# Performance work log

Hardware: AMD Instinct MI355X
Metric: run time of the kernel (lower is better)

## Reference

```python
import jax, jax.numpy as jnp
import numpy as np

N, E = 20000, 320000
EPS = 1e-5
NEG_SLOPE = 0.2


def gat_conv(x, src, dst, W, att_src, att_dst, bias, num_nodes):
    # W: [Fin, H*C], att_*: [H, C], bias: [H*C]
    H, C = att_src.shape
    h = (x @ W).reshape(num_nodes, H, C)            # [N,H,C]
    a_s = jnp.einsum('nhc,hc->nh', h, att_src)      # [N,H]
    a_d = jnp.einsum('nhc,hc->nh', h, att_dst)      # [N,H]
    e = jax.nn.leaky_relu(a_s[src] + a_d[dst], NEG_SLOPE)  # [E,H]
    m = jax.ops.segment_max(e, dst, num_segments=num_nodes)       # per-dst max (self-loops guarantee non-empty)
    ex = jnp.exp(e - m[dst])
    s = jax.ops.segment_sum(ex, dst, num_segments=num_nodes)
    alpha = ex / s[dst]                              # [E,H] segment softmax
    out = jax.ops.segment_sum(h[src] * alpha[:, :, None], dst, num_segments=num_nodes)  # [N,H,C]
    return out.reshape(num_nodes, H * C) + bias


def batch_norm(x, gamma, beta):
    mu = x.mean(axis=0)
    var = x.var(axis=0)  # biased, as torch BN uses for normalization
    return (x - mu) * jax.lax.rsqrt(var + EPS) * gamma + beta


def setup_inputs() -> dict:
    key = jax.random.key(0)
    ks = jax.random.split(key, 32)
    x = jax.random.normal(ks[0], (N, 512), dtype=jnp.float32)
    edge_index = jax.random.randint(ks[1], (2, E), 0, N, dtype=jnp.int32)
    d = {"x": x, "edge_index": edge_index}
    # layer configs: (Fin, C_out, H)
    cfgs = [(512, 64, 8), (512, 64, 4), (256, 64, 2), (128, 16, 1)]
    i = 2
    for li, (fin, c, h) in enumerate(cfgs, start=1):
        sc = 1.0 / np.sqrt(fin)
        d[f"W{li}"] = jax.random.normal(ks[i], (fin, h * c), dtype=jnp.float32) * sc; i += 1
        d[f"as{li}"] = jax.random.normal(ks[i], (h, c), dtype=jnp.float32) * 0.1; i += 1
        d[f"ad{li}"] = jax.random.normal(ks[i], (h, c), dtype=jnp.float32) * 0.1; i += 1
        d[f"b{li}"] = jnp.zeros((h * c,), dtype=jnp.float32)
        if li < 4:
            d[f"g{li}"] = jnp.ones((h * c,), dtype=jnp.float32)
            d[f"be{li}"] = jnp.zeros((h * c,), dtype=jnp.float32)
    return d


def reference(x, edge_index, W1, as1, ad1, b1, g1, be1, W2, as2, ad2, b2, g2, be2, W3, as3, ad3, b3, g3, be3, W4, as4, ad4, b4):
    num_nodes = x.shape[0]
    loop = jnp.arange(num_nodes, dtype=edge_index.dtype)
    src = jnp.concatenate([edge_index[0], loop])  # add_self_loops=True
    dst = jnp.concatenate([edge_index[1], loop])
    h = gat_conv(x, src, dst, W1, as1, ad1, b1, num_nodes)
    h = jax.nn.elu(batch_norm(h, g1, be1))
    h = gat_conv(h, src, dst, W2, as2, ad2, b2, num_nodes)
    h = jax.nn.elu(batch_norm(h, g2, be2))
    h = gat_conv(h, src, dst, W3, as3, ad3, b3, num_nodes)
    h = jax.nn.elu(batch_norm(h, g3, be3))
    h = gat_conv(h, src, dst, W4, as4, ad4, b4, num_nodes)
    return jax.nn.log_softmax(h, axis=1)
```

## Files before the change

kernel.cpp:

```cpp
#include <hip/hip_runtime.h>
#include <hip/hip_bf16.h>
#include <cstdint>
#include <cstddef>

#define NN 20000
#define EE 320000
#define ET (EE + NN)
#define MPAD 20096
#define BNP 256
#define SCHUNK 20

typedef __attribute__((ext_vector_type(8))) short  short8;
typedef __attribute__((ext_vector_type(4))) float  floatx4;

__device__ inline unsigned short f2bf(float f) {
    unsigned u = __float_as_uint(f);
    u += 0x7FFFu + ((u >> 16) & 1u);
    return (unsigned short)(u >> 16);
}
__device__ inline float bf2f(unsigned short b) {
    return __uint_as_float(((unsigned)b) << 16);
}
__device__ inline float bflo(unsigned u) { return __uint_as_float(u << 16); }
__device__ inline float bfhi(unsigned u) { return __uint_as_float(u & 0xFFFF0000u); }

__global__ void zero_i32(int* __restrict__ p, int n) {
    int i = blockIdx.x * blockDim.x + threadIdx.x;
    if (i < n) p[i] = 0;
}

__global__ void cvt_a_bf16(const float* __restrict__ in, unsigned short* __restrict__ out,
                           int M, int Mpad, int K) {
    long long base = ((long long)blockIdx.x * blockDim.x + threadIdx.x) * 4;
    if (base >= (long long)Mpad * K) return;
    int row = (int)(base / K);
    float4 v = make_float4(0.f, 0.f, 0.f, 0.f);
    if (row < M) v = *(const float4*)(in + base);
    ushort4 o;
    o.x = f2bf(v.x); o.y = f2bf(v.y); o.z = f2bf(v.z); o.w = f2bf(v.w);
    *(ushort4*)(out + base) = o;
}

#define W1SZ (512 * 512)
#define W2SZ (512 * 256)
#define W3SZ (256 * 128)
__global__ void cvt_w_all(const float* __restrict__ W1, unsigned short* __restrict__ Wt1,
                          const float* __restrict__ W2, unsigned short* __restrict__ Wt2,
                          const float* __restrict__ W3, unsigned short* __restrict__ Wt3) {
    int i = blockIdx.x * blockDim.x + threadIdx.x;
    const float* W; unsigned short* Wt; int K, N, idx;
    if (i < W1SZ)               { W = W1; Wt = Wt1; K = 512; N = 512; idx = i; }
    else if (i < W1SZ + W2SZ)   { W = W2; Wt = Wt2; K = 512; N = 256; idx = i - W1SZ; }
    else if (i < W1SZ + W2SZ + W3SZ) { W = W3; Wt = Wt3; K = 256; N = 128; idx = i - W1SZ - W2SZ; }
    else return;
    int k = idx / N, n = idx - k * N;
    Wt[(size_t)n * K + k] = f2bf(W[idx]);
}

__global__ void count_edges(const int* __restrict__ dst, int* __restrict__ cnt) {
    int e = blockIdx.x * blockDim.x + threadIdx.x;
    if (e >= ET) return;
    int d = (e < EE) ? dst[e] : (e - EE);
    atomicAdd(&cnt[d], 1);
}

__global__ __launch_bounds__(1024) void scan_fast(const int* __restrict__ cnt,
                                                  int* __restrict__ rowp,
                                                  int* __restrict__ wptr, int n) {
    __shared__ int sums[1024];
    const int t = threadIdx.x;
    const int base = t * SCHUNK;
    int local[SCHUNK];
    int acc = 0;
#pragma unroll
    for (int i = 0; i < SCHUNK; ++i) {
        int idx = base + i;
        int v = (idx < n) ? cnt[idx] : 0;
        local[i] = acc;
        acc += v;
    }
    sums[t] = acc;
    __syncthreads();
    for (int o = 1; o < 1024; o <<= 1) {
        int u = (t >= o) ? sums[t - o] : 0;
        __syncthreads();
        sums[t] += u;
        __syncthreads();
    }
    int excl = sums[t] - acc;
#pragma unroll
    for (int i = 0; i < SCHUNK; ++i) {
        int idx = base + i;
        if (idx < n) { int rp = excl + local[i]; rowp[idx] = rp; wptr[idx] = rp; }
    }
    if (t == 1023) rowp[n] = sums[1023];
}

__global__ void fill_edges(const int* __restrict__ src, const int* __restrict__ dst,
                           int* __restrict__ wptr, int* __restrict__ colx) {
    int e = blockIdx.x * blockDim.x + threadIdx.x;
    if (e >= ET) return;
    int s, d;
    if (e < EE) { s = src[e]; d = dst[e]; } else { s = e - EE; d = e - EE; }
    int pos = atomicAdd(&wptr[d], 1);
    colx[pos] = s;
}

__global__ __launch_bounds__(256) void gemm_bf16_fused(
        const unsigned short* __restrict__ A, const unsigned short* __restrict__ Bt,
        unsigned short* __restrict__ hN, float* __restrict__ aS, float* __restrict__ aD,
        const float* __restrict__ atts, const float* __restrict__ attd,
        int M, int N, int K) {
    __shared__ unsigned short As[128][40];
    __shared__ unsigned short Bs[128][40];
    const int t = threadIdx.x;
    const int lane = t & 63, wave = t >> 6;
    const int wm = wave >> 1, wn = wave & 1;
    const int quad = lane >> 4, mrow = lane & 15;
    const int row0 = blockIdx.y * 128, col0 = blockIdx.x * 128;
    const int srow = t >> 2, schunk = (t & 3) * 8;

    floatx4 acc[4][4];
#pragma unroll
    for (int i = 0; i < 4; ++i)
#pragma unroll
        for (int j = 0; j < 4; ++j)
#pragma unroll
            for (int r = 0; r < 4; ++r) acc[i][j][r] = 0.f;

    for (int k0 = 0; k0 < K; k0 += 32) {
        uint4 ra0 = *(const uint4*)(A  + (size_t)(row0 + srow)      * K + k0 + schunk);
        uint4 ra1 = *(const uint4*)(A  + (size_t)(row0 + srow + 64) * K + k0 + schunk);
        uint4 rb0 = *(const uint4*)(Bt + (size_t)(col0 + srow)      * K + k0 + schunk);
        uint4 rb1 = *(const uint4*)(Bt + (size_t)(col0 + srow + 64) * K + k0 + schunk);
        __syncthreads();
        *(uint4*)&As[srow][schunk]      = ra0;
        *(uint4*)&As[srow + 64][schunk] = ra1;
        *(uint4*)&Bs[srow][schunk]      = rb0;
        *(uint4*)&Bs[srow + 64][schunk] = rb1;
        __syncthreads();

        short8 af[4], bfr[4];
#pragma unroll
        for (int i = 0; i < 4; ++i)
            af[i] = *(const short8*)&As[wm * 64 + i * 16 + mrow][quad * 8];
#pragma unroll
        for (int j = 0; j < 4; ++j)
            bfr[j] = *(const short8*)&Bs[wn * 64 + j * 16 + mrow][quad * 8];
#pragma unroll
        for (int i = 0; i < 4; ++i)
#pragma unroll
            for (int j = 0; j < 4; ++j)
                acc[i][j] = __builtin_amdgcn_mfma_f32_16x16x32_bf16(af[i], bfr[j], acc[i][j], 0, 0, 0);
    }

    const int head = (col0 + wn * 64) >> 6;
    float attS[4], attD[4];
#pragma unroll
    for (int j = 0; j < 4; ++j) {
        attS[j] = atts[head * 64 + j * 16 + mrow];
        attD[j] = attd[head * 64 + j * 16 + mrow];
    }

#pragma unroll
    for (int i = 0; i < 4; ++i) {
#pragma unroll
        for (int r = 0; r < 4; ++r) {
            int row = row0 + wm * 64 + i * 16 + quad * 4 + r;
            float ps = acc[i][0][r] * attS[0] + acc[i][1][r] * attS[1]
                     + acc[i][2][r] * attS[2] + acc[i][3][r] * attS[3];
            float pd = acc[i][0][r] * attD[0] + acc[i][1][r] * attD[1]
                     + acc[i][2][r] * attD[2] + acc[i][3][r] * attD[3];
#pragma unroll
            for (int o = 1; o < 16; o <<= 1) {
                ps += __shfl_xor(ps, o);
                pd += __shfl_xor(pd, o);
            }
            if (row < M) {
                if (mrow == 0) {
                    aS[(size_t)head * M + row] = ps;
                    aD[(size_t)head * M + row] = pd;
                }
#pragma unroll
                for (int j = 0; j < 4; ++j)
                    hN[(size_t)row * N + col0 + wn * 64 + j * 16 + mrow] = f2bf(acc[i][j][r]);
            }
        }
    }
}

template <int HH>
__global__ __launch_bounds__(256) void gat_agg_head32(
        const unsigned short* __restrict__ hN,
        const float* __restrict__ aS, const float* __restrict__ aD,
        const int* __restrict__ rowp, const int* __restrict__ colx,
        const float* __restrict__ bias, float* __restrict__ out, int Nn) {
    constexpr int F = HH * 64;
    constexpr int G = 8 / HH;
    __shared__ uint2 pair[4][4][33];
    const int L = blockIdx.x;
    const int x8 = L & 7;
    const int hd = x8 / G;
    const int nodeblk = (L >> 3) * G + (x8 & (G - 1));
    const int wave = threadIdx.x >> 6, lane = threadIdx.x & 63;
    const int grp = lane >> 4;
    const int q   = lane & 15;
    const int n = nodeblk * 16 + wave * 4 + grp;
    if (n >= Nn) return;

    const float* aSh = aS + (size_t)hd * Nn;
    const float adv = aD[(size_t)hd * Nn + n];
    const int b0 = rowp[n], b1 = rowp[n + 1];
    const unsigned short* hbase = hN + hd * 64;

    float m, s;
    float a0 = 0.f, a1 = 0.f, a2 = 0.f, a3 = 0.f;

    auto gather = [&](int cnt) {
        const int iters = (cnt + 3) >> 2;
        for (int it = 0; it < iters; ++it) {
            const int j = it << 2;
            uint2 x0 = pair[wave][grp][j + 0];
            uint2 x1 = pair[wave][grp][j + 1];
            uint2 x2 = pair[wave][grp][j + 2];
            uint2 x3 = pair[wave][grp][j + 3];
            uint2 v0 = *(const uint2*)(hbase + (size_t)x0.x * F + q * 4);
            uint2 v1 = *(const uint2*)(hbase + (size_t)x1.x * F + q * 4);
            uint2 v2 = *(const uint2*)(hbase + (size_t)x2.x * F + q * 4);
            uint2 v3 = *(const uint2*)(hbase + (size_t)x3.x * F + q * 4);
            float p0 = __uint_as_float(x0.y), p1 = __uint_as_float(x1.y);
            float p2 = __uint_as_float(x2.y), p3 = __uint_as_float(x3.y);
            a0 += p0 * bflo(v0.x) + p1 * bflo(v1.x) + p2 * bflo(v2.x) + p3 * bflo(v3.x);
            a1 += p0 * bfhi(v0.x) + p1 * bfhi(v1.x) + p2 * bfhi(v2.x) + p3 * bfhi(v3.x);
            a2 += p0 * bflo(v0.y) + p1 * bflo(v1.y) + p2 * bflo(v2.y) + p3 * bflo(v3.y);
            a3 += p0 * bfhi(v0.y) + p1 * bfhi(v1.y) + p2 * bfhi(v2.y) + p3 * bfhi(v3.y);
        }
    };

    {
        const int cnt = min(32, b1 - b0);
        int sn0 = 0, sn1 = 0;
        if (q < cnt)      sn0 = colx[b0 + q];
        if (q + 16 < cnt) sn1 = colx[b0 + q + 16];
        float t0 = aSh[sn0] + adv;
        float t1 = aSh[sn1] + adv;
        float e0 = (q < cnt)      ? ((t0 > 0.f) ? t0 : 0.2f * t0) : -1e30f;
        float e1 = (q + 16 < cnt) ? ((t1 > 0.f) ? t1 : 0.2f * t1) : -1e30f;
        float mc = fmaxf(e0, e1);
#pragma unroll
        for (int o = 8; o > 0; o >>= 1) mc = fmaxf(mc, __shfl_xor(mc, o));
        m = mc;
        float p0 = __expf(e0 - m);
        float p1 = __expf(e1 - m);
        float ps = p0 + p1;
#pragma unroll
        for (int o = 8; o > 0; o >>= 1) ps += __shfl_xor(ps, o);
        s = ps;
        pair[wave][grp][q]      = make_uint2((unsigned)sn0, __float_as_uint(p0));
        pair[wave][grp][q + 16] = make_uint2((unsigned)sn1, __float_as_uint(p1));
        __threadfence_block();
        gather(cnt);
    }

    for (int c0 = b0 + 32; c0 < b1; c0 += 32) {
        __threadfence_block();
        const int cnt = min(32, b1 - c0);
        int sn0 = 0, sn1 = 0;
        if (q < cnt)      sn0 = colx[c0 + q];
        if (q + 16 < cnt) sn1 = colx[c0 + q + 16];
        float t0 = aSh[sn0] + adv;
        float t1 = aSh[sn1] + adv;
        float e0 = (q < cnt)      ? ((t0 > 0.f) ? t0 : 0.2f * t0) : -1e30f;
        float e1 = (q + 16 < cnt) ? ((t1 > 0.f) ? t1 : 0.2f * t1) : -1e30f;
        float mc = fmaxf(e0, e1);
#pragma unroll
        for (int o = 8; o > 0; o >>= 1) mc = fmaxf(mc, __shfl_xor(mc, o));
        float nm = fmaxf(m, mc);
        float sc = __expf(m - nm);
        float p0 = __expf(e0 - nm);
        float p1 = __expf(e1 - nm);
        float ps = p0 + p1;
#pragma unroll
        for (int o = 8; o > 0; o >>= 1) ps += __shfl_xor(ps, o);
        s = s * sc + ps;
        a0 *= sc; a1 *= sc; a2 *= sc; a3 *= sc;
        m = nm;
        pair[wave][grp][q]      = make_uint2((unsigned)sn0, __float_as_uint(p0));
        pair[wave][grp][q + 16] = make_uint2((unsigned)sn1, __float_as_uint(p1));
        __threadfence_block();
        gather(cnt);
    }

    const float inv = 1.f / s;
    const int cb = hd * 64 + q * 4;
    float4 o4;
    o4.x = a0 * inv + bias[cb + 0];
    o4.y = a1 * inv + bias[cb + 1];
    o4.z = a2 * inv + bias[cb + 2];
    o4.w = a3 * inv + bias[cb + 3];
    *(float4*)(out + (size_t)n * F + cb) = o4;
}

__global__ __launch_bounds__(256) void gemm_l4_fused(const unsigned short* __restrict__ A,
                                                     const float* __restrict__ B,
                                                     unsigned short* __restrict__ C,
                                                     float* __restrict__ aS, float* __restrict__ aD,
                                                     const float* __restrict__ atts,
                                                     const float* __restrict__ attd,
                                                     int M, int N, int K) {
    __shared__ float As[16][65];
    __shared__ float Bs[16][64];
    const int tid = threadIdx.x;
    const int tx = tid & 15, ty = tid >> 4;
    const int row0 = blockIdx.y * 64, col0 = blockIdx.x * 64;
    const int rA = tid >> 2, kq = (tid & 3) << 2;
    const int rB = tid >> 4, cq = (tid & 15) << 2;
    float acc[4][4] = {};

    for (int k0 = 0; k0 < K; k0 += 16) {
        ushort4 ha = *(const ushort4*)(A + (size_t)(row0 + rA) * K + k0 + kq);
        float4 fb = make_float4(0.f, 0.f, 0.f, 0.f);
        int bcol = col0 + cq;
        if (bcol < N) fb = *(const float4*)(B + (size_t)(k0 + rB) * N + bcol);
        As[kq + 0][rA] = bf2f(ha.x); As[kq + 1][rA] = bf2f(ha.y);
        As[kq + 2][rA] = bf2f(ha.z); As[kq + 3][rA] = bf2f(ha.w);
        *(float4*)&Bs[rB][cq] = fb;
        __syncthreads();
#pragma unroll
        for (int k = 0; k < 16; ++k) {
            float a0 = As[k][ty * 4 + 0];
            float a1 = As[k][ty * 4 + 1];
            float a2 = As[k][ty * 4 + 2];
            float a3 = As[k][ty * 4 + 3];
            float4 b = *(float4*)&Bs[k][tx * 4];
            acc[0][0] += a0 * b.x; acc[0][1] += a0 * b.y; acc[0][2] += a0 * b.z; acc[0][3] += a0 * b.w;
            acc[1][0] += a1 * b.x; acc[1][1] += a1 * b.y; acc[1][2] += a1 * b.z; acc[1][3] += a1 * b.w;
            acc[2][0] += a2 * b.x; acc[2][1] += a2 * b.y; acc[2][2] += a2 * b.z; acc[2][3] += a2 * b.w;
            acc[3][0] += a3 * b.x; acc[3][1] += a3 * b.y; acc[3][2] += a3 * b.z; acc[3][3] += a3 * b.w;
        }
        __syncthreads();
    }
    float as_part[4], ad_part[4];
#pragma unroll
    for (int i = 0; i < 4; ++i) { as_part[i] = 0.f; ad_part[i] = 0.f; }
    if (tx < 4) {
#pragma unroll
        for (int i = 0; i < 4; ++i) {
#pragma unroll
            for (int jj = 0; jj < 4; ++jj) {
                int c = tx * 4 + jj;
                as_part[i] += acc[i][jj] * atts[c];
                ad_part[i] += acc[i][jj] * attd[c];
            }
        }
    }
#pragma unroll
    for (int i = 0; i < 4; ++i) {
        float ps = as_part[i], pd = ad_part[i];
        ps += __shfl_xor(ps, 1); ps += __shfl_xor(ps, 2);
        pd += __shfl_xor(pd, 1); pd += __shfl_xor(pd, 2);
        int r = row0 + ty * 4 + i;
        if (r < M) {
            if (tx == 0) { aS[r] = ps; aD[r] = pd; }
#pragma unroll
            for (int jj = 0; jj < 4; ++jj) {
                int c = col0 + tx * 4 + jj;
                if (c < N) C[(size_t)r * N + c] = f2bf(acc[i][jj]);
            }
        }
    }
}

template <int C>
__global__ void gat_agg_l4_ls(const unsigned short* __restrict__ ht,
                              const float* __restrict__ as, const float* __restrict__ aD,
                              const int* __restrict__ rowp, const int* __restrict__ colx,
                              const float* __restrict__ bias, float* __restrict__ out, int Nn) {
    int n = blockIdx.x * 4 + (threadIdx.x >> 6);
    int lane = threadIdx.x & 63;
    if (n >= Nn) return;
    float adv = aD[n];
    int b0 = rowp[n], b1 = rowp[n + 1];

    float m = -1e30f, s = 0.f, acc = 0.f;
    for (int c0 = b0; c0 < b1; c0 += 64) {
        int cnt = b1 - c0; if (cnt > 64) cnt = 64;
        int sn = 0; float e = -1e30f;
        if (lane < cnt) {
            sn = colx[c0 + lane];
            float tt = as[sn] + adv;
            e = (tt > 0.f) ? tt : 0.2f * tt;
        }
        float mc = e;
#pragma unroll
        for (int o = 32; o > 0; o >>= 1) mc = fmaxf(mc, __shfl_xor(mc, o));
        float nm = fmaxf(m, mc);
        float sc = __expf(m - nm);
        acc *= sc; s *= sc;
        float p = (lane < cnt) ? __expf(e - nm) : 0.f;
        float ps = p;
#pragma unroll
        for (int o = 32; o > 0; o >>= 1) ps += __shfl_xor(ps, o);
        s += ps; m = nm;

        int j = 0;
        for (; j + 4 <= cnt; j += 4) {
            int s0 = __shfl(sn, j),     s1 = __shfl(sn, j + 1);
            int s2 = __shfl(sn, j + 2), s3 = __shfl(sn, j + 3);
            float p0 = __shfl(p, j),     p1 = __shfl(p, j + 1);
            float p2 = __shfl(p, j + 2), p3 = __shfl(p, j + 3);
            float h0 = 0.f, h1 = 0.f, h2 = 0.f, h3 = 0.f;
            if (lane < C) {
                h0 = bf2f(ht[(size_t)s0 * C + lane]);
                h1 = bf2f(ht[(size_t)s1 * C + lane]);
                h2 = bf2f(ht[(size_t)s2 * C + lane]);
                h3 = bf2f(ht[(size_t)s3 * C + lane]);
            }
            acc += p0 * h0 + p1 * h1 + p2 * h2 + p3 * h3;
        }
        for (; j < cnt; ++j) {
            int sj = __shfl(sn, j);
            float pj = __shfl(p, j);
            float hv = (lane < C) ? bf2f(ht[(size_t)sj * C + lane]) : 0.f;
            acc += pj * hv;
        }
    }
    float v = (lane < C) ? (acc / s + bias[lane]) : -1e30f;
    float mx = v;
#pragma unroll
    for (int o = 8; o > 0; o >>= 1) mx = fmaxf(mx, __shfl_xor(mx, o));
    float ex = (lane < C) ? __expf(v - mx) : 0.f;
#pragma unroll
    for (int o = 8; o > 0; o >>= 1) ex += __shfl_xor(ex, o);
    float l = __logf(ex) + mx;
    if (lane < C) out[(size_t)n * C + lane] = v - l;
}

template <int F>
__global__ __launch_bounds__(256) void bn_stats_det(const float* __restrict__ x,
                                                    float* __restrict__ part,
                                                    long long total) {
    constexpr int R  = 1024 / F;
    constexpr int NT = F / 4;
    __shared__ float sd[256 * 9];
    const int t = threadIdx.x;
    long long idx = ((long long)blockIdx.x * 256 + t) * 4;
    const long long stride = (long long)gridDim.x * 1024;
    float s0 = 0, s1 = 0, s2 = 0, s3 = 0, q0 = 0, q1 = 0, q2 = 0, q3 = 0;
    for (; idx < total; idx += stride) {
        float4 v = *(const float4*)(x + idx);
        s0 += v.x; q0 += v.x * v.x;
        s1 += v.y; q1 += v.y * v.y;
        s2 += v.z; q2 += v.z * v.z;
        s3 += v.w; q3 += v.w * v.w;
    }
    sd[t * 9 + 0] = s0; sd[t * 9 + 1] = s1; sd[t * 9 + 2] = s2; sd[t * 9 + 3] = s3;
    sd[t * 9 + 4] = q0; sd[t * 9 + 5] = q1; sd[t * 9 + 6] = q2; sd[t * 9 + 7] = q3;
    __syncthreads();
    if (t < NT) {
        float a[8];
#pragma unroll
        for (int k = 0; k < 8; ++k) a[k] = sd[t * 9 + k];
        for (int r = 1; r < R; ++r)
#pragma unroll
            for (int k = 0; k < 8; ++k) a[k] += sd[(t + r * NT) * 9 + k];
        int col = t * 4;
        float* pb = part + (size_t)blockIdx.x * 2 * F;
#pragma unroll
        for (int k = 0; k < 4; ++k) {
            pb[col + k]     = a[k];
            pb[F + col + k] = a[4 + k];
        }
    }
}

template <int F>
__global__ __launch_bounds__(256) void bn_reduce_par(const float* __restrict__ part,
                                                     const float* __restrict__ gamma,
                                                     const float* __restrict__ beta,
                                                     float* __restrict__ ss,
                                                     float invN) {
    __shared__ float sd[8][33];
    const int t = threadIdx.x;
    const int pr = t >> 5;
    const int tg = t & 31;
    const int c0 = blockIdx.x * 16;
    const int col = (tg < 16) ? (c0 + tg) : (F + c0 + (tg - 16));
    float a = 0.f;
    for (int p = pr; p < BNP; p += 8)
        a += part[(size_t)p * 2 * F + col];
    sd[pr][tg] = a;
    __syncthreads();
    if (pr == 0) {
        float tot = sd[0][tg];
#pragma unroll
        for (int r = 1; r < 8; ++r) tot += sd[r][tg];
        sd[0][tg] = tot;
    }
    __syncthreads();
    if (t < 16) {
        int c = c0 + t;
        float s = sd[0][t];
        float q = sd[0][16 + t];
        float mu = s * invN;
        float var = q * invN - mu * mu;
        float sc = gamma[c] * rsqrtf(var + 1e-5f);
        ss[c] = sc;
        ss[F + c] = beta[c] - mu * sc;
    }
}

__global__ void bn_apply_elu_bf16(const float* __restrict__ x, const float* __restrict__ ss,
                                  unsigned short* __restrict__ outA,
                                  int Nn, int F, int fmask) {
    long long idx4 = ((long long)blockIdx.x * blockDim.x + threadIdx.x) * 4;
    int row = (int)(idx4 / F);
    ushort4 o = make_ushort4(0, 0, 0, 0);
    if (row < Nn) {
        int c = (int)(idx4 & fmask);
        float4 v = *(const float4*)(x + idx4);
        float v0 = v.x * ss[c + 0] + ss[F + c + 0];
        float v1 = v.y * ss[c + 1] + ss[F + c + 1];
        float v2 = v.z * ss[c + 2] + ss[F + c + 2];
        float v3 = v.w * ss[c + 3] + ss[F + c + 3];
        v0 = (v0 > 0.f) ? v0 : (__expf(v0) - 1.f);
        v1 = (v1 > 0.f) ? v1 : (__expf(v1) - 1.f);
        v2 = (v2 > 0.f) ? v2 : (__expf(v2) - 1.f);
        v3 = (v3 > 0.f) ? v3 : (__expf(v3) - 1.f);
        o.x = f2bf(v0); o.y = f2bf(v1); o.z = f2bf(v2); o.w = f2bf(v3);
    }
    *(ushort4*)(outA + idx4) = o;
}

extern "C" void kernel_launch(void* const* d_in, const int* in_sizes, int n_in,
                              void* d_out, int out_size, void* d_ws, size_t ws_size,
                              hipStream_t stream) {
    const float* x   = (const float*)d_in[0];
    const int*   ei  = (const int*)d_in[1];
    const float* W1  = (const float*)d_in[2];
    const float* as1 = (const float*)d_in[3];
    const float* ad1 = (const float*)d_in[4];
    const float* b1  = (const float*)d_in[5];
    const float* ga1 = (const float*)d_in[6];
    const float* be1 = (const float*)d_in[7];
    const float* W2  = (const float*)d_in[8];
    const float* as2 = (const float*)d_in[9];
    const float* ad2 = (const float*)d_in[10];
    const float* b2  = (const float*)d_in[11];
    const float* ga2 = (const float*)d_in[12];
    const float* be2 = (const float*)d_in[13];
    const float* W3  = (const float*)d_in[14];
    const float* as3 = (const float*)d_in[15];
    const float* ad3 = (const float*)d_in[16];
    const float* b3  = (const float*)d_in[17];
    const float* ga3 = (const float*)d_in[18];
    const float* be3 = (const float*)d_in[19];
    const float* W4  = (const float*)d_in[20];
    const float* as4 = (const float*)d_in[21];
    const float* ad4 = (const float*)d_in[22];
    const float* b4  = (const float*)d_in[23];
    float* outp = (float*)d_out;

    uint8_t* base = (uint8_t*)d_ws;
    size_t off = 0;
    auto alloc = [&](size_t nbytes) -> void* {
        off = (off + 255) & ~(size_t)255;
        void* p = base + off;
        off += nbytes;
        return p;
    };
    float* bufO = (float*)alloc((size_t)NN * 512 * 4);
    unsigned short* bufA = (unsigned short*)alloc((size_t)MPAD * 512 * 2);
    unsigned short* hN   = (unsigned short*)alloc((size_t)NN * 512 * 2);
    unsigned short* Wt1  = (unsigned short*)alloc((size_t)512 * 512 * 2);
    unsigned short* Wt2  = (unsigned short*)alloc((size_t)256 * 512 * 2);
    unsigned short* Wt3  = (unsigned short*)alloc((size_t)128 * 256 * 2);
    float* aSn  = (float*)alloc((size_t)NN * 8 * 4);
    float* aDn  = (float*)alloc((size_t)NN * 8 * 4);
    int*   cnt  = (int*)alloc((size_t)NN * 4);
    int*   rowp = (int*)alloc((size_t)(NN + 1) * 4);
    int*   wptr = (int*)alloc((size_t)NN * 4);
    int*   colx = (int*)alloc((size_t)ET * 4);
    float* bnp  = (float*)alloc((size_t)BNP * 1024 * 4);
    float* bns  = (float*)alloc((size_t)1024 * 4);

    const int* srcRow = ei;
    const int* dstRow = ei + EE;

    zero_i32<<<(NN + 255) / 256, 256, 0, stream>>>(cnt, NN);
    count_edges<<<(ET + 255) / 256, 256, 0, stream>>>(dstRow, cnt);
    scan_fast<<<1, 1024, 0, stream>>>(cnt, rowp, wptr, NN);
    fill_edges<<<(ET + 255) / 256, 256, 0, stream>>>(srcRow, dstRow, wptr, colx);

    cvt_w_all<<<(W1SZ + W2SZ + W3SZ) / 256, 256, 0, stream>>>(W1, Wt1, W2, Wt2, W3, Wt3);

    const int NBLK = (NN + 15) / 16;

    {
        cvt_a_bf16<<<((MPAD * 512 / 4) + 255) / 256, 256, 0, stream>>>(x, bufA, NN, MPAD, 512);
        dim3 g(512 / 128, MPAD / 128);
        gemm_bf16_fused<<<g, 256, 0, stream>>>(bufA, Wt1, hN, aSn, aDn, as1, ad1, NN, 512, 512);
        gat_agg_head32<8><<<NBLK * 8, 256, 0, stream>>>(hN, aSn, aDn, rowp, colx, b1, bufO, NN);
        bn_stats_det<512><<<BNP, 256, 0, stream>>>(bufO, bnp, (long long)NN * 512);
        bn_reduce_par<512><<<512 / 16, 256, 0, stream>>>(bnp, ga1, be1, bns, 1.0f / NN);
        bn_apply_elu_bf16<<<(MPAD * 512 / 4) / 256, 256, 0, stream>>>(bufO, bns, bufA, NN, 512, 511);
    }
    {
        dim3 g(256 / 128, MPAD / 128);
        gemm_bf16_fused<<<g, 256, 0, stream>>>(bufA, Wt2, hN, aSn, aDn, as2, ad2, NN, 256, 512);
        gat_agg_head32<4><<<((NBLK + 1) / 2) * 8, 256, 0, stream>>>(hN, aSn, aDn, rowp, colx, b2, bufO, NN);
        bn_stats_det<256><<<BNP, 256, 0, stream>>>(bufO, bnp, (long long)NN * 256);
        bn_reduce_par<256><<<256 / 16, 256, 0, stream>>>(bnp, ga2, be2, bns, 1.0f / NN);
        bn_apply_elu_bf16<<<(MPAD * 256 / 4) / 256, 256, 0, stream>>>(bufO, bns, bufA, NN, 256, 255);
    }
    {
        dim3 g(128 / 128, MPAD / 128);
        gemm_bf16_fused<<<g, 256, 0, stream>>>(bufA, Wt3, hN, aSn, aDn, as3, ad3, NN, 128, 256);
        gat_agg_head32<2><<<((NBLK + 3) / 4) * 8, 256, 0, stream>>>(hN, aSn, aDn, rowp, colx, b3, bufO, NN);
        bn_stats_det<128><<<BNP, 256, 0, stream>>>(bufO, bnp, (long long)NN * 128);
        bn_reduce_par<128><<<128 / 16, 256, 0, stream>>>(bnp, ga3, be3, bns, 1.0f / NN);
        bn_apply_elu_bf16<<<(MPAD * 128 / 4) / 256, 256, 0, stream>>>(bufO, bns, bufA, NN, 128, 127);
    }
    {
        dim3 g(1, (NN + 63) / 64);
        gemm_l4_fused<<<g, 256, 0, stream>>>(bufA, W4, hN, aSn, aDn, as4, ad4, NN, 16, 128);
        gat_agg_l4_ls<16><<<(NN + 3) / 4, 256, 0, stream>>>(hN, aSn, aDn, rowp, colx, b4, outp, NN);
    }
}
```

Measured before the change: 440.3 us.

## Fuse BatchNorm partial statistics into GAT aggregation kernel epilogue

The aggregation kernel now reduces per-column sums and sums of squares of its output tile across its waves and writes per-block partials, removing the separate bn_stats pass that re-read the full fp32 activation. The BN reduce kernel is reworked to sum these per-block, per-head partials with a head/group indexing scheme. This trades an extra full-tensor read for a block-wide __syncthreads plus shuffles in the aggregation kernel and a larger partial buffer (about 10k blocks x 128 floats) that the reduce kernel must walk.

```diff
diff --git a/kernel.cpp b/kernel.cpp
--- a/kernel.cpp
+++ b/kernel.cpp
@@ -7,7 +7,6 @@
 #define EE 320000
 #define ET (EE + NN)
 #define MPAD 20096
-#define BNP 256
 #define SCHUNK 20
 
 typedef __attribute__((ext_vector_type(8))) short  short8;
@@ -194,10 +193,12 @@
         const unsigned short* __restrict__ hN,
         const float* __restrict__ aS, const float* __restrict__ aD,
         const int* __restrict__ rowp, const int* __restrict__ colx,
-        const float* __restrict__ bias, float* __restrict__ out, int Nn) {
+        const float* __restrict__ bias, float* __restrict__ out,
+        float* __restrict__ part, int Nn) {
     constexpr int F = HH * 64;
     constexpr int G = 8 / HH;
     __shared__ uint2 pair[4][4][33];
+    __shared__ float red[4][16][8];
     const int L = blockIdx.x;
     const int x8 = L & 7;
     const int hd = x8 / G;
@@ -206,99 +207,131 @@
     const int grp = lane >> 4;
     const int q   = lane & 15;
     const int n = nodeblk * 16 + wave * 4 + grp;
-    if (n >= Nn) return;
-
-    const float* aSh = aS + (size_t)hd * Nn;
-    const float adv = aD[(size_t)hd * Nn + n];
-    const int b0 = rowp[n], b1 = rowp[n + 1];
-    const unsigned short* hbase = hN + hd * 64;
-
-    float m, s;
-    float a0 = 0.f, a1 = 0.f, a2 = 0.f, a3 = 0.f;
-
-    auto gather = [&](int cnt) {
-        const int iters = (cnt + 3) >> 2;
-        for (int it = 0; it < iters; ++it) {
-            const int j = it << 2;
-            uint2 x0 = pair[wave][grp][j + 0];
-            uint2 x1 = pair[wave][grp][j + 1];
-            uint2 x2 = pair[wave][grp][j + 2];
-            uint2 x3 = pair[wave][grp][j + 3];
-            uint2 v0 = *(const uint2*)(hbase + (size_t)x0.x * F + q * 4);
-            uint2 v1 = *(const uint2*)(hbase + (size_t)x1.x * F + q * 4);
-            uint2 v2 = *(const uint2*)(hbase + (size_t)x2.x * F + q * 4);
-            uint2 v3 = *(const uint2*)(hbase + (size_t)x3.x * F + q * 4);
-            float p0 = __uint_as_float(x0.y), p1 = __uint_as_float(x1.y);
-            float p2 = __uint_as_float(x2.y), p3 = __uint_as_float(x3.y);
-            a0 += p0 * bflo(v0.x) + p1 * bflo(v1.x) + p2 * bflo(v2.x) + p3 * bflo(v3.x);
-            a1 += p0 * bfhi(v0.x) + p1 * bfhi(v1.x) + p2 * bfhi(v2.x) + p3 * bfhi(v3.x);
-            a2 += p0 * bflo(v0.y) + p1 * bflo(v1.y) + p2 * bflo(v2.y) + p3 * bflo(v3.y);
-            a3 += p0 * bfhi(v0.y) + p1 * bfhi(v1.y) + p2 * bfhi(v2.y) + p3 * bfhi(v3.y);
-        }
-    };
-
-    {
-        const int cnt = min(32, b1 - b0);
-        int sn0 = 0, sn1 = 0;
-        if (q < cnt)      sn0 = colx[b0 + q];
-        if (q + 16 < cnt) sn1 = colx[b0 + q + 16];
-        float t0 = aSh[sn0] + adv;
-        float t1 = aSh[sn1] + adv;
-        float e0 = (q < cnt)      ? ((t0 > 0.f) ? t0 : 0.2f * t0) : -1e30f;
-        float e1 = (q + 16 < cnt) ? ((t1 > 0.f) ? t1 : 0.2f * t1) : -1e30f;
-        float mc = fmaxf(e0, e1);
-#pragma unroll
-        for (int o = 8; o > 0; o >>= 1) mc = fmaxf(mc, __shfl_xor(mc, o));
-        m = mc;
-        float p0 = __expf(e0 - m);
-        float p1 = __expf(e1 - m);
-        float ps = p0 + p1;
-#pragma unroll
-        for (int o = 8; o > 0; o >>= 1) ps += __shfl_xor(ps, o);
-        s = ps;
-        pair[wave][grp][q]      = make_uint2((unsigned)sn0, __float_as_uint(p0));
-        pair[wave][grp][q + 16] = make_uint2((unsigned)sn1, __float_as_uint(p1));
-        __threadfence_block();
-        gather(cnt);
-    }
-
-    for (int c0 = b0 + 32; c0 < b1; c0 += 32) {
-        __threadfence_block();
-        const int cnt = min(32, b1 - c0);
-        int sn0 = 0, sn1 = 0;
-        if (q < cnt)      sn0 = colx[c0 + q];
-        if (q + 16 < cnt) sn1 = colx[c0 + q + 16];
-        float t0 = aSh[sn0] + adv;
-        float t1 = aSh[sn1] + adv;
-        float e0 = (q < cnt)      ? ((t0 > 0.f) ? t0 : 0.2f * t0) : -1e30f;
-        float e1 = (q + 16 < cnt) ? ((t1 > 0.f) ? t1 : 0.2f * t1) : -1e30f;
-        float mc = fmaxf(e0, e1);
-#pragma unroll
-        for (int o = 8; o > 0; o >>= 1) mc = fmaxf(mc, __shfl_xor(mc, o));
-        float nm = fmaxf(m, mc);
-        float sc = __expf(m - nm);
-        float p0 = __expf(e0 - nm);
-        float p1 = __expf(e1 - nm);
-        float ps = p0 + p1;
-#pragma unroll
-        for (int o = 8; o > 0; o >>= 1) ps += __shfl_xor(ps, o);
-        s = s * sc + ps;
-        a0 *= sc; a1 *= sc; a2 *= sc; a3 *= sc;
-        m = nm;
-        pair[wave][grp][q]      = make_uint2((unsigned)sn0, __float_as_uint(p0));
-        pair[wave][grp][q + 16] = make_uint2((unsigned)sn1, __float_as_uint(p1));
-        __threadfence_block();
-        gather(cnt);
-    }
-
-    const float inv = 1.f / s;
-    const int cb = hd * 64 + q * 4;
-    float4 o4;
-    o4.x = a0 * inv + bias[cb + 0];
-    o4.y = a1 * inv + bias[cb + 1];
-    o4.z = a2 * inv + bias[cb + 2];
-    o4.w = a3 * inv + bias[cb + 3];
-    *(float4*)(out + (size_t)n * F + cb) = o4;
+    const bool valid = (n < Nn);
+
+    float4 o4 = make_float4(0.f, 0.f, 0.f, 0.f);
+
+    if (valid) {
+        const float* aSh = aS + (size_t)hd * Nn;
+        const float adv = aD[(size_t)hd * Nn + n];
+        const int b0 = rowp[n], b1 = rowp[n + 1];
+        const unsigned short* hbase = hN + hd * 64;
+
+        float m, s;
+        float a0 = 0.f, a1 = 0.f, a2 = 0.f, a3 = 0.f;
+
+        auto gather = [&](int cnt) {
+            const int iters = (cnt + 3) >> 2;
+            for (int it = 0; it < iters; ++it) {
+                const int j = it << 2;
+                uint2 x0 = pair[wave][grp][j + 0];
+                uint2 x1 = pair[wave][grp][j + 1];
+                uint2 x2 = pair[wave][grp][j + 2];
+                uint2 x3 = pair[wave][grp][j + 3];
+                uint2 v0 = *(const uint2*)(hbase + (size_t)x0.x * F + q * 4);
+                uint2 v1 = *(const uint2*)(hbase + (size_t)x1.x * F + q * 4);
+                uint2 v2 = *(const uint2*)(hbase + (size_t)x2.x * F + q * 4);
+                uint2 v3 = *(const uint2*)(hbase + (size_t)x3.x * F + q * 4);
+                float p0 = __uint_as_float(x0.y), p1 = __uint_as_float(x1.y);
+                float p2 = __uint_as_float(x2.y), p3 = __uint_as_float(x3.y);
+                a0 += p0 * bflo(v0.x) + p1 * bflo(v1.x) + p2 * bflo(v2.x) + p3 * bflo(v3.x);
+                a1 += p0 * bfhi(v0.x) + p1 * bfhi(v1.x) + p2 * bfhi(v2.x) + p3 * bfhi(v3.x);
+                a2 += p0 * bflo(v0.y) + p1 * bflo(v1.y) + p2 * bflo(v2.y) + p3 * bflo(v3.y);
+                a3 += p0 * bfhi(v0.y) + p1 * bfhi(v1.y) + p2 * bfhi(v2.y) + p3 * bfhi(v3.y);
+            }
+        };
+
+        {
+            const int cnt = min(32, b1 - b0);
+            int sn0 = 0, sn1 = 0;
+            if (q < cnt)      sn0 = colx[b0 + q];
+            if (q + 16 < cnt) sn1 = colx[b0 + q + 16];
+            float t0 = aSh[sn0] + adv;
+            float t1 = aSh[sn1] + adv;
+            float e0 = (q < cnt)      ? ((t0 > 0.f) ? t0 : 0.2f * t0) : -1e30f;
+            float e1 = (q + 16 < cnt) ? ((t1 > 0.f) ? t1 : 0.2f * t1) : -1e30f;
+            float mc = fmaxf(e0, e1);
+#pragma unroll
+            for (int o = 8; o > 0; o >>= 1) mc = fmaxf(mc, __shfl_xor(mc, o));
+            m = mc;
+            float p0 = __expf(e0 - m);
+            float p1 = __expf(e1 - m);
+            float ps = p0 + p1;
+#pragma unroll
+            for (int o = 8; o > 0; o >>= 1) ps += __shfl_xor(ps, o);
+            s = ps;
+            pair[wave][grp][q]      = make_uint2((unsigned)sn0, __float_as_uint(p0));
+            pair[wave][grp][q + 16] = make_uint2((unsigned)sn1, __float_as_uint(p1));
+            __threadfence_block();
+            gather(cnt);
+        }
+
+        for (int c0 = b0 + 32; c0 < b1; c0 += 32) {
+            __threadfence_block();
+            const int cnt = min(32, b1 - c0);
+            int sn0 = 0, sn1 = 0;
+            if (q < cnt)      sn0 = colx[c0 + q];
+            if (q + 16 < cnt) sn1 = colx[c0 + q + 16];
+            float t0 = aSh[sn0] + adv;
+            float t1 = aSh[sn1] + adv;
+            float e0 = (q < cnt)      ? ((t0 > 0.f) ? t0 : 0.2f * t0) : -1e30f;
+            float e1 = (q + 16 < cnt) ? ((t1 > 0.f) ? t1 : 0.2f * t1) : -1e30f;
+            float mc = fmaxf(e0, e1);
+#pragma unroll
+            for (int o = 8; o > 0; o >>= 1) mc = fmaxf(mc, __shfl_xor(mc, o));
+            float nm = fmaxf(m, mc);
+            float sc = __expf(m - nm);
+            float p0 = __expf(e0 - nm);
+            float p1 = __expf(e1 - nm);
+            float ps = p0 + p1;
+#pragma unroll
+            for (int o = 8; o > 0; o >>= 1) ps += __shfl_xor(ps, o);
+            s = s * sc + ps;
+            a0 *= sc; a1 *= sc; a2 *= sc; a3 *= sc;
+            m = nm;
+            pair[wave][grp][q]      = make_uint2((unsigned)sn0, __float_as_uint(p0));
+            pair[wave][grp][q + 16] = make_uint2((unsigned)sn1, __float_as_uint(p1));
+            __threadfence_block();
+            gather(cnt);
+        }
+
+        const float inv = 1.f / s;
+        const int cb = hd * 64 + q * 4;
+        o4.x = a0 * inv + bias[cb + 0];
+        o4.y = a1 * inv + bias[cb + 1];
+        o4.z = a2 * inv + bias[cb + 2];
+        o4.w = a3 * inv + bias[cb + 3];
+        *(float4*)(out + (size_t)n * F + cb) = o4;
+    }
+
+    float s0 = o4.x, s1 = o4.y, s2 = o4.z, s3 = o4.w;
+    float q0 = s0 * s0, q1 = s1 * s1, q2 = s2 * s2, q3 = s3 * s3;
+#pragma unroll
+    for (int o = 16; o < 64; o <<= 1) {
+        s0 += __shfl_xor(s0, o); s1 += __shfl_xor(s1, o);
+        s2 += __shfl_xor(s2, o); s3 += __shfl_xor(s3, o);
+        q0 += __shfl_xor(q0, o); q1 += __shfl_xor(q1, o);
+        q2 += __shfl_xor(q2, o); q3 += __shfl_xor(q3, o);
+    }
+    if (grp == 0) {
+        red[wave][q][0] = s0; red[wave][q][1] = s1;
+        red[wave][q][2] = s2; red[wave][q][3] = s3;
+        red[wave][q][4] = q0; red[wave][q][5] = q1;
+        red[wave][q][6] = q2; red[wave][q][7] = q3;
+    }
+    __syncthreads();
+    if (wave == 0 && lane < 16) {
+        float a[8];
+#pragma unroll
+        for (int k = 0; k < 8; ++k)
+            a[k] = red[0][q][k] + red[1][q][k] + red[2][q][k] + red[3][q][k];
+        float* pb = part + (size_t)L * 128;
+#pragma unroll
+        for (int k = 0; k < 4; ++k) {
+            pb[q * 4 + k]      = a[k];
+            pb[64 + q * 4 + k] = a[4 + k];
+        }
+    }
 }
 
 __global__ __launch_bounds__(256) void gemm_l4_fused(const unsigned short* __restrict__ A,
@@ -437,58 +470,26 @@
 }
 
 template <int F>
-__global__ __launch_bounds__(256) void bn_stats_det(const float* __restrict__ x,
-                                                    float* __restrict__ part,
-                                                    long long total) {
-    constexpr int R  = 1024 / F;
-    constexpr int NT = F / 4;
-    __shared__ float sd[256 * 9];
-    const int t = threadIdx.x;
-    long long idx = ((long long)blockIdx.x * 256 + t) * 4;
-    const long long stride = (long long)gridDim.x * 1024;
-    float s0 = 0, s1 = 0, s2 = 0, s3 = 0, q0 = 0, q1 = 0, q2 = 0, q3 = 0;
-    for (; idx < total; idx += stride) {
-        float4 v = *(const float4*)(x + idx);
-        s0 += v.x; q0 += v.x * v.x;
-        s1 += v.y; q1 += v.y * v.y;
-        s2 += v.z; q2 += v.z * v.z;
-        s3 += v.w; q3 += v.w * v.w;
-    }
-    sd[t * 9 + 0] = s0; sd[t * 9 + 1] = s1; sd[t * 9 + 2] = s2; sd[t * 9 + 3] = s3;
-    sd[t * 9 + 4] = q0; sd[t * 9 + 5] = q1; sd[t * 9 + 6] = q2; sd[t * 9 + 7] = q3;
-    __syncthreads();
-    if (t < NT) {
-        float a[8];
-#pragma unroll
-        for (int k = 0; k < 8; ++k) a[k] = sd[t * 9 + k];
-        for (int r = 1; r < R; ++r)
-#pragma unroll
-            for (int k = 0; k < 8; ++k) a[k] += sd[(t + r * NT) * 9 + k];
-        int col = t * 4;
-        float* pb = part + (size_t)blockIdx.x * 2 * F;
-#pragma unroll
-        for (int k = 0; k < 4; ++k) {
-            pb[col + k]     = a[k];
-            pb[F + col + k] = a[4 + k];
-        }
-    }
-}
-
-template <int F>
 __global__ __launch_bounds__(256) void bn_reduce_par(const float* __restrict__ part,
                                                      const float* __restrict__ gamma,
                                                      const float* __restrict__ beta,
                                                      float* __restrict__ ss,
-                                                     float invN) {
+                                                     float invN, int NB8) {
+    constexpr int G = 512 / F;
     __shared__ float sd[8][33];
     const int t = threadIdx.x;
     const int pr = t >> 5;
     const int tg = t & 31;
     const int c0 = blockIdx.x * 16;
-    const int col = (tg < 16) ? (c0 + tg) : (F + c0 + (tg - 16));
+    const int c  = c0 + (tg & 15);
+    const int hd = c >> 6;
+    const int off = (c & 63) + ((tg < 16) ? 0 : 64);
     float a = 0.f;
-    for (int p = pr; p < BNP; p += 8)
-        a += part[(size_t)p * 2 * F + col];
+    for (int g = 0; g < G; ++g) {
+        const float* pb = part + (size_t)(hd * G + g) * 128 + off;
+        for (int j = pr; j < NB8; j += 8)
+            a += pb[(size_t)j * 8 * 128];
+    }
     sd[pr][tg] = a;
     __syncthreads();
     if (pr == 0) {
@@ -499,14 +500,14 @@
     }
     __syncthreads();
     if (t < 16) {
-        int c = c0 + t;
+        int cc = c0 + t;
         float s = sd[0][t];
         float q = sd[0][16 + t];
         float mu = s * invN;
         float var = q * invN - mu * mu;
-        float sc = gamma[c] * rsqrtf(var + 1e-5f);
-        ss[c] = sc;
-        ss[F + c] = beta[c] - mu * sc;
+        float sc = gamma[cc] * rsqrtf(var + 1e-5f);
+        ss[cc] = sc;
+        ss[F + cc] = beta[cc] - mu * sc;
     }
 }
 
@@ -581,7 +582,7 @@
     int*   rowp = (int*)alloc((size_t)(NN + 1) * 4);
     int*   wptr = (int*)alloc((size_t)NN * 4);
     int*   colx = (int*)alloc((size_t)ET * 4);
-    float* bnp  = (float*)alloc((size_t)BNP * 1024 * 4);
+    float* bnp  = (float*)alloc((size_t)10048 * 128 * 4);
     float* bns  = (float*)alloc((size_t)1024 * 4);
 
     const int* srcRow = ei;
@@ -600,25 +601,24 @@
         cvt_a_bf16<<<((MPAD * 512 / 4) + 255) / 256, 256, 0, stream>>>(x, bufA, NN, MPAD, 512);
         dim3 g(512 / 128, MPAD / 128);
         gemm_bf16_fused<<<g, 256, 0, stream>>>(bufA, Wt1, hN, aSn, aDn, as1, ad1, NN, 512, 512);
-        gat_agg_head32<8><<<NBLK * 8, 256, 0, stream>>>(hN, aSn, aDn, rowp, colx, b1, bufO, NN);
-        bn_stats_det<512><<<BNP, 256, 0, stream>>>(bufO, bnp, (long long)NN * 512);
-        bn_reduce_par<512><<<512 / 16, 256, 0, stream>>>(bnp, ga1, be1, bns, 1.0f / NN);
+        gat_agg_head32<8><<<NBLK * 8, 256, 0, stream>>>(hN, aSn, aDn, rowp, colx, b1, bufO, bnp, NN);
+        bn_reduce_par<512><<<512 / 16, 256, 0, stream>>>(bnp, ga1, be1, bns, 1.0f / NN, NBLK);
         bn_apply_elu_bf16<<<(MPAD * 512 / 4) / 256, 256, 0, stream>>>(bufO, bns, bufA, NN, 512, 511);
     }
     {
         dim3 g(256 / 128, MPAD / 128);
         gemm_bf16_fused<<<g, 256, 0, stream>>>(bufA, Wt2, hN, aSn, aDn, as2, ad2, NN, 256, 512);
-        gat_agg_head32<4><<<((NBLK + 1) / 2) * 8, 256, 0, stream>>>(hN, aSn, aDn, rowp, colx, b2, bufO, NN);
-        bn_stats_det<256><<<BNP, 256, 0, stream>>>(bufO, bnp, (long long)NN * 256);
-        bn_reduce_par<256><<<256 / 16, 256, 0, stream>>>(bnp, ga2, be2, bns, 1.0f / NN);
+        const int nb8 = (NBLK + 1) / 2;
+        gat_agg_head32<4><<<nb8 * 8, 256, 0, stream>>>(hN, aSn, aDn, rowp, colx, b2, bufO, bnp, NN);
+        bn_reduce_par<256><<<256 / 16, 256, 0, stream>>>(bnp, ga2, be2, bns, 1.0f / NN, nb8);
         bn_apply_elu_bf16<<<(MPAD * 256 / 4) / 256, 256, 0, stream>>>(bufO, bns, bufA, NN, 256, 255);
     }
     {
         dim3 g(128 / 128, MPAD / 128);
         gemm_bf16_fused<<<g, 256, 0, stream>>>(bufA, Wt3, hN, aSn, aDn, as3, ad3, NN, 128, 256);
-        gat_agg_head32<2><<<((NBLK + 3) / 4) * 8, 256, 0, stream>>>(hN, aSn, aDn, rowp, colx, b3, bufO, NN);
-        bn_stats_det<128><<<BNP, 256, 0, stream>>>(bufO, bnp, (long long)NN * 128);
-        bn_reduce_par<128><<<128 / 16, 256, 0, stream>>>(bnp, ga3, be3, bns, 1.0f / NN);
+        const int nb8 = (NBLK + 3) / 4;
+        gat_agg_head32<2><<<nb8 * 8, 256, 0, stream>>>(hN, aSn, aDn, rowp, colx, b3, bufO, bnp, NN);
+        bn_reduce_par<128><<<128 / 16, 256, 0, stream>>>(bnp, ga3, be3, bns, 1.0f / NN, nb8);
         bn_apply_elu_bf16<<<(MPAD * 128 / 4) / 256, 256, 0, stream>>>(bufO, bns, bufA, NN, 128, 127);
     }
     {
```

Result: slower. 531.8 us (+20.8%).
